# Performance work log

Measured on AMD Instinct MI355X. Metric: run time of the kernel, lower is better.

## Reference

```python
import jax, jax.numpy as jnp
import numpy as np

B, N, M, D = 256, 256, 256, 4
PID_MAX = 5

def setup_inputs() -> dict:
    key = jax.random.key(0)
    k1, k2, k3, k4 = jax.random.split(key, 4)
    return {
        "target": jax.random.normal(k1, (B, N, D), dtype=jnp.float32),
        "reco": jax.random.normal(k2, (B, M, D), dtype=jnp.float32),
        "in_pid": jax.random.randint(k3, (B, N), 0, PID_MAX),
        "out_pid": jax.random.randint(k4, (B, M), 0, PID_MAX),
    }

def reference(target, reco, in_pid, out_pid):
    dt = target.dtype
    mask_x = in_pid != 0   # [B, N] valid (non-zero-pid) target particles
    mask_y = out_pid != 0  # [B, M] valid reco particles
    fx = mask_x.astype(dt)
    fy = mask_y.astype(dt)
    n_in = jnp.maximum(jnp.asarray(1.0, dt), fx.sum(-1))    # [B]
    n_out = jnp.maximum(jnp.asarray(1.0, dt), fy.sum(-1))   # [B]

    # pairwise Euclidean distances between valid points; invalid pairs -> +inf
    diff = target[:, :, None, :] - reco[:, None, :, :]       # [B, N, M, D]
    dist = jnp.sqrt(jnp.sum(diff * diff, axis=-1))           # [B, N, M]
    pair_mask = mask_x[:, :, None] & mask_y[:, None, :]
    dist_m = jnp.where(pair_mask, dist, jnp.inf)

    min_xy = jnp.min(dist_m, axis=-1)                        # [B, N] nearest reco per target
    min_yx = jnp.min(dist_m, axis=-2)                        # [B, M] nearest target per reco
    sum_xy = jnp.sum(jnp.where(mask_x, min_xy, 0.0), axis=-1)
    sum_yx = jnp.sum(jnp.where(mask_y, min_yx, 0.0), axis=-1)
    normal = 0.5 * (sum_xy / n_out + sum_yx / n_in)          # [B]

    # edge cases matching the torch branches:
    # if no valid reco: sum ||x_nonzero|| / n_in ; elif no valid target: 0
    x_norms = jnp.linalg.norm(target, axis=-1)               # [B, N]
    fallback = jnp.sum(jnp.where(mask_x, x_norms, 0.0), axis=-1) / n_in
    has_x = mask_x.any(-1)
    has_y = mask_y.any(-1)
    per_nonzero = jnp.where(~has_y, fallback,
                            jnp.where(~has_x, jnp.asarray(0.0, dt), normal))

    # zero-pid reco particles: mean norm (denominator clamped to >=1)
    y_norms = jnp.linalg.norm(reco, axis=-1)                 # [B, M]
    n_y_zero = jnp.maximum(jnp.asarray(1.0, dt), (1.0 - fy).sum(-1))
    per_zero = jnp.sum(jnp.where(~mask_y, y_norms, 0.0), axis=-1) / n_y_zero

    eucl_non_zero = jnp.mean(per_nonzero)
    eucl_zero = jnp.mean(per_zero)
    return (eucl_non_zero, eucl_zero)
```

## Files before the change

### kernel.cpp

```cpp
#include <hip/hip_runtime.h>
#include <math.h>

#define B_ 256
#define N_ 256
#define M_ 256
#define P_ 8
#define ROWS_P 32

__device__ inline float wave_sum(float v) {
    v += __shfl_down(v, 32, 64);
    v += __shfl_down(v, 16, 64);
    v += __shfl_down(v, 8, 64);
    v += __shfl_down(v, 4, 64);
    v += __shfl_down(v, 2, 64);
    v += __shfl_down(v, 1, 64);
    return v;
}

__device__ inline float dist2(const float4 a, const float4 r) {
    const float dx = a.x - r.x;
    const float dy = a.y - r.y;
    const float dz = a.z - r.z;
    const float dw = a.w - r.w;
    return fmaf(dx, dx, fmaf(dy, dy, fmaf(dz, dz, dw * dw)));
}

__global__ __launch_bounds__(256, 4) void chamfer_part_kernel(
    const float4* __restrict__ target,
    const float4* __restrict__ reco,
    const int*    __restrict__ in_pid,
    const int*    __restrict__ out_pid,
    float*        __restrict__ ws)
{
    const int bp = blockIdx.x;
    const int b  = bp >> 3;
    const int p  = bp & 7;
    const int t  = threadIdx.x;

    __shared__ float4 s_t[N_];
    __shared__ float4 s_r[M_];
    __shared__ float  s_mx[N_];
    __shared__ float  s_my[M_];
    __shared__ float  partials[4][6];

    const float4 tx = target[b * N_ + t];
    const float4 rx = reco  [b * M_ + t];
    const bool mx = (in_pid [b * N_ + t] != 0);
    const bool my = (out_pid[b * M_ + t] != 0);

    const float SENT = 1e18f;
    s_t[t]  = mx ? tx : make_float4(SENT, SENT, SENT, SENT);
    s_r[t]  = my ? rx : make_float4(SENT, SENT, SENT, SENT);
    s_mx[t] = mx ? 1.0f : 0.0f;
    s_my[t] = my ? 1.0f : 0.0f;
    __syncthreads();

    const int g   = t >> 5;
    const int mc  = t & 31;
    const int row = p * ROWS_P + g * 4;

    const float4 a0 = s_t[row + 0];
    const float4 a1 = s_t[row + 1];
    const float4 a2 = s_t[row + 2];
    const float4 a3 = s_t[row + 3];
    float am0 = 3.0e38f, am1 = 3.0e38f, am2 = 3.0e38f, am3 = 3.0e38f;
    #pragma unroll
    for (int i = 0; i < 8; ++i) {
        const float4 r = s_r[i * 32 + mc];
        am0 = fminf(am0, dist2(a0, r));
        am1 = fminf(am1, dist2(a1, r));
        am2 = fminf(am2, dist2(a2, r));
        am3 = fminf(am3, dist2(a3, r));
    }
    #pragma unroll
    for (int off = 16; off >= 1; off >>= 1) {
        am0 = fminf(am0, __shfl_xor(am0, off, 64));
        am1 = fminf(am1, __shfl_xor(am1, off, 64));
        am2 = fminf(am2, __shfl_xor(am2, off, 64));
        am3 = fminf(am3, __shfl_xor(am3, off, 64));
    }
    float c_sxy = 0.0f;
    if (mc == 0) {
        c_sxy = s_mx[row + 0] * sqrtf(am0) + s_mx[row + 1] * sqrtf(am1)
              + s_mx[row + 2] * sqrtf(am2) + s_mx[row + 3] * sqrtf(am3);
    }

    const float4 b0 = s_r[row + 0];
    const float4 b1 = s_r[row + 1];
    const float4 b2 = s_r[row + 2];
    const float4 b3 = s_r[row + 3];
    float bm0 = 3.0e38f, bm1 = 3.0e38f, bm2 = 3.0e38f, bm3 = 3.0e38f;
    #pragma unroll
    for (int i = 0; i < 8; ++i) {
        const float4 q = s_t[i * 32 + mc];
        bm0 = fminf(bm0, dist2(b0, q));
        bm1 = fminf(bm1, dist2(b1, q));
        bm2 = fminf(bm2, dist2(b2, q));
        bm3 = fminf(bm3, dist2(b3, q));
    }
    #pragma unroll
    for (int off = 16; off >= 1; off >>= 1) {
        bm0 = fminf(bm0, __shfl_xor(bm0, off, 64));
        bm1 = fminf(bm1, __shfl_xor(bm1, off, 64));
        bm2 = fminf(bm2, __shfl_xor(bm2, off, 64));
        bm3 = fminf(bm3, __shfl_xor(bm3, off, 64));
    }
    float c_syx = 0.0f;
    if (mc == 0) {
        c_syx = s_my[row + 0] * sqrtf(bm0) + s_my[row + 1] * sqrtf(bm1)
              + s_my[row + 2] * sqrtf(bm2) + s_my[row + 3] * sqrtf(bm3);
    }

    float c_fx = 0.0f, c_fy = 0.0f, c_xn = 0.0f, c_yz = 0.0f;
    if ((t >> 5) == p) {
        if (mx) {
            c_fx = 1.0f;
            c_xn = sqrtf(fmaf(tx.x, tx.x, fmaf(tx.y, tx.y, fmaf(tx.z, tx.z, tx.w * tx.w))));
        }
        if (my) {
            c_fy = 1.0f;
        } else {
            c_yz = sqrtf(fmaf(rx.x, rx.x, fmaf(rx.y, rx.y, fmaf(rx.z, rx.z, rx.w * rx.w))));
        }
    }

    const int wave = t >> 6;
    const int lane = t & 63;
    const float r0 = wave_sum(c_sxy);
    const float r1 = wave_sum(c_syx);
    const float r2 = wave_sum(c_fx);
    const float r3 = wave_sum(c_fy);
    const float r4 = wave_sum(c_xn);
    const float r5 = wave_sum(c_yz);
    if (lane == 0) {
        partials[wave][0] = r0;
        partials[wave][1] = r1;
        partials[wave][2] = r2;
        partials[wave][3] = r3;
        partials[wave][4] = r4;
        partials[wave][5] = r5;
    }
    __syncthreads();
    if (t == 0) {
        float s0 = 0.f, s1 = 0.f, s2 = 0.f, s3 = 0.f, s4 = 0.f, s5 = 0.f;
        #pragma unroll
        for (int w = 0; w < 4; ++w) {
            s0 += partials[w][0];
            s1 += partials[w][1];
            s2 += partials[w][2];
            s3 += partials[w][3];
            s4 += partials[w][4];
            s5 += partials[w][5];
        }
        float* o = ws + bp * 8;
        o[0] = s0; o[1] = s1; o[2] = s2; o[3] = s3; o[4] = s4; o[5] = s5;
    }
}

__global__ __launch_bounds__(256) void chamfer_final_kernel(
    const float* __restrict__ ws, float* __restrict__ out)
{
    const int t = threadIdx.x;
    float sxy = 0.f, syx = 0.f, fx = 0.f, fy = 0.f, xn = 0.f, yz = 0.f;
    #pragma unroll
    for (int p = 0; p < P_; ++p) {
        const float* w = ws + ((t << 3) + p) * 8;
        sxy += w[0]; syx += w[1]; fx += w[2]; fy += w[3]; xn += w[4]; yz += w[5];
    }
    const float n_in   = fmaxf(1.0f, fx);
    const float n_out  = fmaxf(1.0f, fy);
    const bool  has_x  = (fx > 0.0f);
    const bool  has_y  = (fy > 0.0f);
    const float normal   = 0.5f * (sxy / n_out + syx / n_in);
    const float fallback = xn / n_in;
    const float per_nz   = (!has_y) ? fallback : ((!has_x) ? 0.0f : normal);
    const float n_y_zero = fmaxf(1.0f, (float)M_ - fy);
    const float per_z    = yz / n_y_zero;

    const float a = wave_sum(per_nz);
    const float z = wave_sum(per_z);
    __shared__ float pa[4], pz[4];
    const int wave = t >> 6;
    const int lane = t & 63;
    if (lane == 0) { pa[wave] = a; pz[wave] = z; }
    __syncthreads();
    if (t == 0) {
        out[0] = (pa[0] + pa[1] + pa[2] + pa[3]) * (1.0f / (float)B_);
        out[1] = (pz[0] + pz[1] + pz[2] + pz[3]) * (1.0f / (float)B_);
    }
}

extern "C" void kernel_launch(void* const* d_in, const int* in_sizes, int n_in,
                              void* d_out, int out_size, void* d_ws, size_t ws_size,
                              hipStream_t stream) {
    const float4* target  = (const float4*)d_in[0];
    const float4* reco    = (const float4*)d_in[1];
    const int*    in_pid  = (const int*)d_in[2];
    const int*    out_pid = (const int*)d_in[3];
    float*        out     = (float*)d_out;
    float*        ws      = (float*)d_ws;

    chamfer_part_kernel<<<B_ * P_, 256, 0, stream>>>(target, reco, in_pid, out_pid, ws);
    chamfer_final_kernel<<<1, 256, 0, stream>>>(ws, out);
}
```

Baseline: 76.24 us.

## Fuse partial and final kernels into one 1024-thread block per batch with atomics

Replaces the two-kernel scheme (8 blocks per batch writing partials, then a single-block final reduction) with one kernel launching a 1024-thread block per batch that computes all rows and finishes the per-batch math in-block. Batch results are combined with float atomicAdd into the output, which is zeroed by a memset first. This removes the second launch and the workspace round-trip, and staging is no longer repeated across eight blocks. In exchange it launches fewer blocks (256 instead of 2048), which may lower occupancy, and float atomics make the final sum order nondeterministic.

```diff
diff --git a/kernel.cpp b/kernel.cpp
--- a/kernel.cpp
+++ b/kernel.cpp
@@ -4,8 +4,6 @@
 #define B_ 256
 #define N_ 256
 #define M_ 256
-#define P_ 8
-#define ROWS_P 32
 
 __device__ inline float wave_sum(float v) {
     v += __shfl_down(v, 32, 64);
@@ -25,39 +23,51 @@
     return fmaf(dx, dx, fmaf(dy, dy, fmaf(dz, dz, dw * dw)));
 }
 
-__global__ __launch_bounds__(256, 4) void chamfer_part_kernel(
+__global__ __launch_bounds__(1024, 4) void chamfer_full_kernel(
     const float4* __restrict__ target,
     const float4* __restrict__ reco,
     const int*    __restrict__ in_pid,
     const int*    __restrict__ out_pid,
-    float*        __restrict__ ws)
+    float*        __restrict__ out)
 {
-    const int bp = blockIdx.x;
-    const int b  = bp >> 3;
-    const int p  = bp & 7;
-    const int t  = threadIdx.x;
+    const int b = blockIdx.x;
+    const int t = threadIdx.x;
 
     __shared__ float4 s_t[N_];
     __shared__ float4 s_r[M_];
     __shared__ float  s_mx[N_];
     __shared__ float  s_my[M_];
-    __shared__ float  partials[4][6];
-
-    const float4 tx = target[b * N_ + t];
-    const float4 rx = reco  [b * M_ + t];
-    const bool mx = (in_pid [b * N_ + t] != 0);
-    const bool my = (out_pid[b * M_ + t] != 0);
+    __shared__ float  partials[16][6];
 
     const float SENT = 1e18f;
-    s_t[t]  = mx ? tx : make_float4(SENT, SENT, SENT, SENT);
-    s_r[t]  = my ? rx : make_float4(SENT, SENT, SENT, SENT);
-    s_mx[t] = mx ? 1.0f : 0.0f;
-    s_my[t] = my ? 1.0f : 0.0f;
+
+    float c_fx = 0.f, c_fy = 0.f, c_xn = 0.f, c_yz = 0.f;
+    if (t < N_) {
+        const float4 v = target[b * N_ + t];
+        const bool m = (in_pid[b * N_ + t] != 0);
+        s_t[t]  = m ? v : make_float4(SENT, SENT, SENT, SENT);
+        s_mx[t] = m ? 1.f : 0.f;
+        if (m) {
+            c_fx = 1.f;
+            c_xn = sqrtf(fmaf(v.x, v.x, fmaf(v.y, v.y, fmaf(v.z, v.z, v.w * v.w))));
+        }
+    } else if (t < N_ + M_) {
+        const int r = t - N_;
+        const float4 v = reco[b * M_ + r];
+        const bool m = (out_pid[b * M_ + r] != 0);
+        s_r[r]  = m ? v : make_float4(SENT, SENT, SENT, SENT);
+        s_my[r] = m ? 1.f : 0.f;
+        if (m) {
+            c_fy = 1.f;
+        } else {
+            c_yz = sqrtf(fmaf(v.x, v.x, fmaf(v.y, v.y, fmaf(v.z, v.z, v.w * v.w))));
+        }
+    }
     __syncthreads();
 
-    const int g   = t >> 5;
-    const int mc  = t & 31;
-    const int row = p * ROWS_P + g * 4;
+    const int c   = t & 15;
+    const int g   = t >> 4;
+    const int row = g * 4;
 
     const float4 a0 = s_t[row + 0];
     const float4 a1 = s_t[row + 1];
@@ -65,22 +75,22 @@
     const float4 a3 = s_t[row + 3];
     float am0 = 3.0e38f, am1 = 3.0e38f, am2 = 3.0e38f, am3 = 3.0e38f;
     #pragma unroll
-    for (int i = 0; i < 8; ++i) {
-        const float4 r = s_r[i * 32 + mc];
+    for (int i = 0; i < 16; ++i) {
+        const float4 r = s_r[i * 16 + c];
         am0 = fminf(am0, dist2(a0, r));
         am1 = fminf(am1, dist2(a1, r));
         am2 = fminf(am2, dist2(a2, r));
         am3 = fminf(am3, dist2(a3, r));
     }
     #pragma unroll
-    for (int off = 16; off >= 1; off >>= 1) {
+    for (int off = 8; off >= 1; off >>= 1) {
         am0 = fminf(am0, __shfl_xor(am0, off, 64));
         am1 = fminf(am1, __shfl_xor(am1, off, 64));
         am2 = fminf(am2, __shfl_xor(am2, off, 64));
         am3 = fminf(am3, __shfl_xor(am3, off, 64));
     }
-    float c_sxy = 0.0f;
-    if (mc == 0) {
+    float c_sxy = 0.f;
+    if (c == 0) {
         c_sxy = s_mx[row + 0] * sqrtf(am0) + s_mx[row + 1] * sqrtf(am1)
               + s_mx[row + 2] * sqrtf(am2) + s_mx[row + 3] * sqrtf(am3);
     }
@@ -91,37 +101,24 @@
     const float4 b3 = s_r[row + 3];
     float bm0 = 3.0e38f, bm1 = 3.0e38f, bm2 = 3.0e38f, bm3 = 3.0e38f;
     #pragma unroll
-    for (int i = 0; i < 8; ++i) {
-        const float4 q = s_t[i * 32 + mc];
+    for (int i = 0; i < 16; ++i) {
+        const float4 q = s_t[i * 16 + c];
         bm0 = fminf(bm0, dist2(b0, q));
         bm1 = fminf(bm1, dist2(b1, q));
         bm2 = fminf(bm2, dist2(b2, q));
         bm3 = fminf(bm3, dist2(b3, q));
     }
     #pragma unroll
-    for (int off = 16; off >= 1; off >>= 1) {
+    for (int off = 8; off >= 1; off >>= 1) {
         bm0 = fminf(bm0, __shfl_xor(bm0, off, 64));
         bm1 = fminf(bm1, __shfl_xor(bm1, off, 64));
         bm2 = fminf(bm2, __shfl_xor(bm2, off, 64));
         bm3 = fminf(bm3, __shfl_xor(bm3, off, 64));
     }
-    float c_syx = 0.0f;
-    if (mc == 0) {
+    float c_syx = 0.f;
+    if (c == 0) {
         c_syx = s_my[row + 0] * sqrtf(bm0) + s_my[row + 1] * sqrtf(bm1)
               + s_my[row + 2] * sqrtf(bm2) + s_my[row + 3] * sqrtf(bm3);
-    }
-
-    float c_fx = 0.0f, c_fy = 0.0f, c_xn = 0.0f, c_yz = 0.0f;
-    if ((t >> 5) == p) {
-        if (mx) {
-            c_fx = 1.0f;
-            c_xn = sqrtf(fmaf(tx.x, tx.x, fmaf(tx.y, tx.y, fmaf(tx.z, tx.z, tx.w * tx.w))));
-        }
-        if (my) {
-            c_fy = 1.0f;
-        } else {
-            c_yz = sqrtf(fmaf(rx.x, rx.x, fmaf(rx.y, rx.y, fmaf(rx.z, rx.z, rx.w * rx.w))));
-        }
     }
 
     const int wave = t >> 6;
@@ -141,52 +138,30 @@
         partials[wave][5] = r5;
     }
     __syncthreads();
+
     if (t == 0) {
-        float s0 = 0.f, s1 = 0.f, s2 = 0.f, s3 = 0.f, s4 = 0.f, s5 = 0.f;
+        float sxy = 0.f, syx = 0.f, fx = 0.f, fy = 0.f, xn = 0.f, yz = 0.f;
         #pragma unroll
-        for (int w = 0; w < 4; ++w) {
-            s0 += partials[w][0];
-            s1 += partials[w][1];
-            s2 += partials[w][2];
-            s3 += partials[w][3];
-            s4 += partials[w][4];
-            s5 += partials[w][5];
+        for (int w = 0; w < 16; ++w) {
+            sxy += partials[w][0];
+            syx += partials[w][1];
+            fx  += partials[w][2];
+            fy  += partials[w][3];
+            xn  += partials[w][4];
+            yz  += partials[w][5];
         }
-        float* o = ws + bp * 8;
-        o[0] = s0; o[1] = s1; o[2] = s2; o[3] = s3; o[4] = s4; o[5] = s5;
-    }
-}
+        const float n_in   = fmaxf(1.0f, fx);
+        const float n_out  = fmaxf(1.0f, fy);
+        const bool  has_x  = (fx > 0.0f);
+        const bool  has_y  = (fy > 0.0f);
+        const float normal   = 0.5f * (sxy / n_out + syx / n_in);
+        const float fallback = xn / n_in;
+        const float per_nz   = (!has_y) ? fallback : ((!has_x) ? 0.0f : normal);
+        const float n_y_zero = fmaxf(1.0f, (float)M_ - fy);
+        const float per_z    = yz / n_y_zero;
 
-__global__ __launch_bounds__(256) void chamfer_final_kernel(
-    const float* __restrict__ ws, float* __restrict__ out)
-{
-    const int t = threadIdx.x;
-    float sxy = 0.f, syx = 0.f, fx = 0.f, fy = 0.f, xn = 0.f, yz = 0.f;
-    #pragma unroll
-    for (int p = 0; p < P_; ++p) {
-        const float* w = ws + ((t << 3) + p) * 8;
-        sxy += w[0]; syx += w[1]; fx += w[2]; fy += w[3]; xn += w[4]; yz += w[5];
-    }
-    const float n_in   = fmaxf(1.0f, fx);
-    const float n_out  = fmaxf(1.0f, fy);
-    const bool  has_x  = (fx > 0.0f);
-    const bool  has_y  = (fy > 0.0f);
-    const float normal   = 0.5f * (sxy / n_out + syx / n_in);
-    const float fallback = xn / n_in;
-    const float per_nz   = (!has_y) ? fallback : ((!has_x) ? 0.0f : normal);
-    const float n_y_zero = fmaxf(1.0f, (float)M_ - fy);
-    const float per_z    = yz / n_y_zero;
-
-    const float a = wave_sum(per_nz);
-    const float z = wave_sum(per_z);
-    __shared__ float pa[4], pz[4];
-    const int wave = t >> 6;
-    const int lane = t & 63;
-    if (lane == 0) { pa[wave] = a; pz[wave] = z; }
-    __syncthreads();
-    if (t == 0) {
-        out[0] = (pa[0] + pa[1] + pa[2] + pa[3]) * (1.0f / (float)B_);
-        out[1] = (pz[0] + pz[1] + pz[2] + pz[3]) * (1.0f / (float)B_);
+        atomicAdd(&out[0], per_nz * (1.0f / (float)B_));
+        atomicAdd(&out[1], per_z  * (1.0f / (float)B_));
     }
 }
 
@@ -198,8 +173,7 @@
     const int*    in_pid  = (const int*)d_in[2];
     const int*    out_pid = (const int*)d_in[3];
     float*        out     = (float*)d_out;
-    float*        ws      = (float*)d_ws;
 
-    chamfer_part_kernel<<<B_ * P_, 256, 0, stream>>>(target, reco, in_pid, out_pid, ws);
-    chamfer_final_kernel<<<1, 256, 0, stream>>>(ws, out);
+    hipMemsetAsync(out, 0, (size_t)out_size * sizeof(float), stream);
+    chamfer_full_kernel<<<B_, 1024, 0, stream>>>(target, reco, in_pid, out_pid, out);
 }
```

New measurement: 75.57 us. No clear change (-0.9%).
